# Performance work log

Measured on AMD Instinct MI355X. Metric: run time of the kernel, lower is better.

Reference implementation:

```python
import jax, jax.numpy as jnp
import numpy as np

N = 20000      # nodes
E = 320000     # edges (before self-loops)
F_IN = 50      # PPI num_features
C1 = 256       # per-head channels, conv1/conv2
H1 = 4         # heads, conv1/conv2
C3 = 121       # PPI num_classes, conv3 per-head channels
H3 = 6         # heads, conv3 (concat=False -> mean)


def gat_conv(x, src, dst, W, a_src, a_dst, b, heads, ch, concat, n):
    """PyG-style GATConv with self-loops already included in (src, dst).
    Messages flow src -> dst; softmax is over incoming edges of each dst node."""
    h = (x @ W).reshape(n, heads, ch)                      # [N, H, C]
    es = jnp.sum(h * a_src, axis=-1)                       # [N, H]
    ed = jnp.sum(h * a_dst, axis=-1)                       # [N, H]
    e = jax.nn.leaky_relu(es[src] + ed[dst], 0.2)          # [E', H]
    m = jax.ops.segment_max(e, dst, num_segments=n)        # stable softmax per dst
    e = jnp.exp(e - m[dst])
    denom = jax.ops.segment_sum(e, dst, num_segments=n)
    alpha = e / jnp.maximum(denom[dst], 1e-16)             # [E', H]
    out = jax.ops.segment_sum(alpha[:, :, None] * h[src], dst, num_segments=n)  # [N, H, C]
    out = out.reshape(n, heads * ch) if concat else out.mean(axis=1)
    return out + b


def setup_inputs() -> dict:
    key = jax.random.key(0)
    ks = jax.random.split(key, 16)

    def p(k, shape, fan_in):
        return (jax.random.normal(k, shape, jnp.float32) / np.float32(np.sqrt(fan_in)))

    x = jax.random.normal(ks[0], (N, F_IN), jnp.float32)
    edge_index = jax.random.randint(ks[1], (2, E), 0, N, dtype=jnp.int64)
    D1 = H1 * C1  # 1024
    return dict(
        x=x, edge_index=edge_index,
        W1=p(ks[2], (F_IN, D1), F_IN), a1s=p(ks[3], (H1, C1), C1), a1d=p(ks[4], (H1, C1), C1), b1=jnp.zeros((D1,), jnp.float32),
        Wl1=p(ks[5], (F_IN, D1), F_IN), bl1=jnp.zeros((D1,), jnp.float32),
        W2=p(ks[6], (D1, D1), D1), a2s=p(ks[7], (H1, C1), C1), a2d=p(ks[8], (H1, C1), C1), b2=jnp.zeros((D1,), jnp.float32),
        Wl2=p(ks[9], (D1, D1), D1), bl2=jnp.zeros((D1,), jnp.float32),
        W3=p(ks[10], (D1, H3 * C3), D1), a3s=p(ks[11], (H3, C3), C3), a3d=p(ks[12], (H3, C3), C3), b3=jnp.zeros((C3,), jnp.float32),
        Wl3=p(ks[13], (D1, C3), D1), bl3=jnp.zeros((C3,), jnp.float32),
    )


def reference(x, edge_index, W1, a1s, a1d, b1, Wl1, bl1, W2, a2s, a2d, b2, Wl2, bl2, W3, a3s, a3d, b3, Wl3, bl3):
    n = x.shape[0]
    loop = jnp.arange(n, dtype=edge_index.dtype)           # PyG GATConv adds self-loops
    src = jnp.concatenate([edge_index[0], loop])
    dst = jnp.concatenate([edge_index[1], loop])
    x1 = jax.nn.elu(gat_conv(x, src, dst, W1, a1s, a1d, b1, H1, C1, True, n) + x @ Wl1 + bl1)
    x2 = jax.nn.elu(gat_conv(x1, src, dst, W2, a2s, a2d, b2, H1, C1, True, n) + x1 @ Wl2 + bl2)
    out = gat_conv(x2, src, dst, W3, a3s, a3d, b3, H3, C3, False, n) + x2 @ Wl3 + bl3
    return out
```

## Files before the change

kernel.cpp:

```cpp
#include <hip/hip_runtime.h>
#include <hip/hip_bf16.h>
#include <math.h>

typedef __bf16 bf16;
typedef __attribute__((ext_vector_type(4))) __bf16 bf16x4;
typedef __attribute__((ext_vector_type(8))) __bf16 bf16x8;
typedef __attribute__((ext_vector_type(4))) float f32x4;

#define N_NODES 20000
#define N_EDGES 320000
#define E2 (N_EDGES + N_NODES)
#define F_IN 50
#define D1 1024
#define NP12 2048
#define NP3 1024
#define SG 2048
#define KA 320

#define PO_A1S 0
#define PO_A1D 1024
#define PO_B1  2048
#define PO_BL1 3072
#define PO_A2S 4096
#define PO_A2D 5120
#define PO_B2  6144
#define PO_BL2 7168
#define PO_A3S 8192
#define PO_A3D 8918
#define PO_B3  9644
#define PO_BL3 9765
#define PO_END 9886

__device__ __forceinline__ int clampi(int v, int lo, int hi)
{
    return v < lo ? lo : (v > hi ? hi : v);
}

__device__ __forceinline__ float loadf(const void* p, long idx, int isb)
{
    return isb ? (float)((const bf16*)p)[idx] : ((const float*)p)[idx];
}

__device__ __forceinline__ int loadei(const int* ei, long idx, int i64)
{
    return i64 ? ei[2 * idx] : ei[idx];
}

__global__ void k_detect(const int* __restrict__ ei,
                         const unsigned short* __restrict__ xw,
                         int* __restrict__ flags)
{
    if (blockIdx.x != 0 || threadIdx.x != 0) return;
    int allz = 1;
    for (int i = 0; i < 128; ++i)
        if (ei[2 * i + 1] != 0) { allz = 0; break; }
    int inr = 0;
    for (int i = 0; i < 128; ++i) {
        int e = (xw[2 * i] >> 7) & 0xFF;
        if (e >= 100 && e <= 140) inr++;
    }
    flags[0] = allz;
    flags[1] = (inr >= 64) ? 1 : 0;
}

template <bool BACT>
__global__ __launch_bounds__(256) void k_gemm(const bf16* __restrict__ A,
                                              const bf16* __restrict__ Bt,
                                              bf16* __restrict__ C,
                                              int M, int K, int lda, int ldb, int ldc,
                                              int mtiles, int ntiles,
                                              const bf16* __restrict__ bias)
{
    __shared__ bf16 As[128 * 64];
    __shared__ bf16 Bs[128 * 64];

    int id = blockIdx.x;
    int gfull = mtiles >> 3;
    int base  = gfull * 8 * ntiles;
    int x, y;
    if (id < base) {
        int gsz = 8 * ntiles;
        int g = id / gsz;
        int r = id - g * gsz;
        x = g * 8 + (r & 7);
        y = r >> 3;
    } else {
        int rem = mtiles - (gfull << 3);
        int r = id - base;
        x = (gfull << 3) + r % rem;
        y = r / rem;
    }
    const int m0 = x * 128;
    const int n0 = y * 128;

    const int tid  = threadIdx.x;
    const int wave = tid >> 6;
    const int lane = tid & 63;
    const int wm   = (wave >> 1) * 64;
    const int wn   = (wave & 1) * 64;
    const int frow  = lane & 15;

    const int srow = wave * 32 + (lane >> 3);
    const int scol = (((lane & 7) ^ (lane >> 3)) * 8);

    f32x4 acc[4][4];
#pragma unroll
    for (int i = 0; i < 4; ++i)
#pragma unroll
        for (int j = 0; j < 4; ++j)
#pragma unroll
            for (int r = 0; r < 4; ++r) acc[i][j][r] = 0.f;

    for (int k0 = 0; k0 < K; k0 += 64) {
#pragma unroll
        for (int i = 0; i < 4; ++i) {
            int ra = srow + i * 8;
            int ga = m0 + ra; if (ga > M - 1) ga = M - 1;
            __builtin_amdgcn_global_load_lds(
                (const __attribute__((address_space(1))) void*)(A + (size_t)ga * lda + k0 + scol),
                (__attribute__((address_space(3))) void*)(As + wave * 2048 + i * 512),
                16, 0, 0);
            int gb = n0 + ra;
            __builtin_amdgcn_global_load_lds(
                (const __attribute__((address_space(1))) void*)(Bt + (size_t)gb * ldb + k0 + scol),
                (__attribute__((address_space(3))) void*)(Bs + wave * 2048 + i * 512),
                16, 0, 0);
        }
        __syncthreads();
#pragma unroll
        for (int kk = 0; kk < 2; ++kk) {
            const int coff = (((kk * 4 + (lane >> 4)) ^ (frow & 7)) << 3);
            bf16x8 af[4], bfr[4];
#pragma unroll
            for (int i = 0; i < 4; ++i) {
                af[i]  = *(const bf16x8*)(As + (wm + i * 16 + frow) * 64 + coff);
                bfr[i] = *(const bf16x8*)(Bs + (wn + i * 16 + frow) * 64 + coff);
            }
#pragma unroll
            for (int i = 0; i < 4; ++i)
#pragma unroll
                for (int j = 0; j < 4; ++j)
                    acc[i][j] = __builtin_amdgcn_mfma_f32_16x16x32_bf16(af[i], bfr[j], acc[i][j], 0, 0, 0);
        }
        __syncthreads();
    }

#pragma unroll
    for (int i = 0; i < 4; ++i) {
#pragma unroll
        for (int j = 0; j < 4; ++j) {
            int rbase = m0 + wm + i * 16 + (lane >> 4) * 4;
            int col   = n0 + wn + j * 16 + frow;
            if constexpr (BACT) {
                float bv = (float)bias[col];
#pragma unroll
                for (int r = 0; r < 4; ++r) {
                    int row = rbase + r;
                    if (row < M) {
                        float v = acc[i][j][r] + bv;
                        v = (v > 0.f) ? v : (__expf(v) - 1.f);
                        C[(size_t)row * ldc + col] = (bf16)v;
                    }
                }
            } else {
#pragma unroll
                for (int r = 0; r < 4; ++r) {
                    int row = rbase + r;
                    if (row < M) C[(size_t)row * ldc + col] = (bf16)acc[i][j][r];
                }
            }
        }
    }
}

__global__ __launch_bounds__(512, 2) void k_gemm256(const bf16* __restrict__ A,
                                                    const bf16* __restrict__ Bt,
                                                    bf16* __restrict__ C,
                                                    int M, int K, int lda, int ldb, int ldc,
                                                    int mtiles, int ntiles)
{
    __shared__ bf16 As[2][256 * 64];
    __shared__ bf16 Bs[2][256 * 64];

    int id = blockIdx.x;
    int gfull = mtiles >> 3;
    int base  = gfull * 8 * ntiles;
    int x, y;
    if (id < base) {
        int gsz = 8 * ntiles;
        int g = id / gsz;
        int r = id - g * gsz;
        x = g * 8 + (r & 7);
        y = r >> 3;
    } else {
        int rem = mtiles - (gfull << 3);
        int r = id - base;
        x = (gfull << 3) + r % rem;
        y = r / rem;
    }
    const int m0 = x * 256;
    const int n0 = y * 256;

    const int tid  = threadIdx.x;
    const int wave = tid >> 6;
    const int lane = tid & 63;
    const int wr   = wave >> 2;
    const int wc   = wave & 3;
    const int frow = lane & 15;
    const int hi   = lane >> 4;
    const int sr8  = lane >> 3;
    const int scol = (((lane & 7) ^ sr8) << 3);

    auto stage_a = [&](int b, int h, int t1) {
        const int k0s = t1 << 6;
#pragma unroll
        for (int i_ = 0; i_ < 2; ++i_) {
            int row_ = h * 128 + i_ * 64 + wave * 8 + sr8;
            int ga_ = m0 + row_; if (ga_ > M - 1) ga_ = M - 1;
            __builtin_amdgcn_global_load_lds(
                (const __attribute__((address_space(1))) void*)(A + (size_t)ga_ * lda + k0s + scol),
                (__attribute__((address_space(3))) void*)(&As[b][(h * 128 + i_ * 64 + wave * 8) * 64]),
                16, 0, 0);
        }
    };
    auto stage_b = [&](int b, int h, int t1) {
        const int k0s = t1 << 6;
#pragma unroll
        for (int i_ = 0; i_ < 2; ++i_) {
            int row_ = h * 128 + i_ * 64 + wave * 8 + sr8;
            int gb_ = n0 + row_;
            __builtin_amdgcn_global_load_lds(
                (const __attribute__((address_space(1))) void*)(Bt + (size_t)gb_ * ldb + k0s + scol),
                (__attribute__((address_space(3))) void*)(&Bs[b][(h * 128 + i_ * 64 + wave * 8) * 64]),
                16, 0, 0);
        }
    };

    f32x4 acc[8][4];
#pragma unroll
    for (int i = 0; i < 8; ++i)
#pragma unroll
        for (int j = 0; j < 4; ++j)
#pragma unroll
            for (int r = 0; r < 4; ++r) acc[i][j][r] = 0.f;

    auto compute = [&](int b, int MH, int NH) {
        bf16x8 af[4][2], bv[2][2];
#pragma unroll
        for (int m_ = 0; m_ < 4; ++m_)
#pragma unroll
            for (int kk_ = 0; kk_ < 2; ++kk_)
                af[m_][kk_] = *(const bf16x8*)&As[b][
                    (wr * 128 + MH * 64 + m_ * 16 + frow) * 64 +
                    (((kk_ * 4 + hi) ^ (frow & 7)) << 3)];
#pragma unroll
        for (int n_ = 0; n_ < 2; ++n_)
#pragma unroll
            for (int kk_ = 0; kk_ < 2; ++kk_)
                bv[n_][kk_] = *(const bf16x8*)&Bs[b][
                    (wc * 64 + NH * 32 + n_ * 16 + frow) * 64 +
                    (((kk_ * 4 + hi) ^ (frow & 7)) << 3)];
        __builtin_amdgcn_s_setprio(1);
#pragma unroll
        for (int kk_ = 0; kk_ < 2; ++kk_)
#pragma unroll
            for (int m_ = 0; m_ < 4; ++m_)
#pragma unroll
                for (int n_ = 0; n_ < 2; ++n_)
                    acc[MH * 4 + m_][NH * 2 + n_] =
                        __builtin_amdgcn_mfma_f32_16x16x32_bf16(
                            af[m_][kk_], bv[n_][kk_],
                            acc[MH * 4 + m_][NH * 2 + n_], 0, 0, 0);
        __builtin_amdgcn_s_setprio(0);
    };

    stage_a(0, 0, 0);
    stage_b(0, 0, 0);
    stage_b(0, 1, 0);
    stage_a(0, 1, 0);

    const int nt = K >> 6;
    int p = 0;
#pragma unroll 1
    for (int t = 0; t < nt - 1; ++t, p ^= 1) {
        stage_a(p ^ 1, 0, t + 1);
        asm volatile("s_waitcnt vmcnt(2)" ::: "memory");
        __builtin_amdgcn_s_barrier();
        compute(p, 0, 0);
        __builtin_amdgcn_s_barrier();
        stage_b(p ^ 1, 0, t + 1);
        compute(p, 0, 1);
        __builtin_amdgcn_s_barrier();
        stage_b(p ^ 1, 1, t + 1);
        compute(p, 1, 1);
        __builtin_amdgcn_s_barrier();
        stage_a(p ^ 1, 1, t + 1);
        compute(p, 1, 0);
        __builtin_amdgcn_s_barrier();
    }
    asm volatile("s_waitcnt vmcnt(0)" ::: "memory");
    __builtin_amdgcn_s_barrier();
    compute(p, 0, 0);
    compute(p, 0, 1);
    compute(p, 1, 1);
    compute(p, 1, 0);

#pragma unroll
    for (int mf = 0; mf < 8; ++mf) {
#pragma unroll
        for (int nf = 0; nf < 4; ++nf) {
            int row0 = m0 + wr * 128 + mf * 16 + hi * 4;
            int col  = n0 + wc * 64 + nf * 16 + frow;
#pragma unroll
            for (int r = 0; r < 4; ++r) {
                int row = row0 + r;
                if (row < M) C[(size_t)row * ldc + col] = (bf16)acc[mf][nf][r];
            }
        }
    }
}

__global__ void k_padx(const void* __restrict__ x, bf16* __restrict__ A2,
                       const int* __restrict__ flags)
{
    int idx = blockIdx.x * 256 + threadIdx.x;
    if (idx >= N_NODES * 64) return;
    int isb = flags[1];
    int n = idx >> 6, k = idx & 63;
    A2[(size_t)n * KA + 256 + k] = (k < F_IN) ? (bf16)loadf(x, (long)n * F_IN + k, isb)
                                              : (bf16)0.f;
}

__global__ __launch_bounds__(256) void k_veca(const void* __restrict__ W1,
                                              const void* __restrict__ a1s,
                                              const void* __restrict__ a1d,
                                              const void* __restrict__ b1,
                                              const void* __restrict__ bl1,
                                              float* __restrict__ ws, float* __restrict__ wd,
                                              bf16* __restrict__ bsum,
                                              const int* __restrict__ flags)
{
    const int isb = flags[1];
    const int k = blockIdx.x;
    const int h = threadIdx.x >> 6;
    const int c0 = threadIdx.x & 63;
    float s = 0.f, d = 0.f;
    if (k < F_IN) {
        for (int c = c0; c < 256; c += 64) {
            float wv = loadf(W1, (long)k * D1 + h * 256 + c, isb);
            s += wv * loadf(a1s, h * 256 + c, isb);
            d += wv * loadf(a1d, h * 256 + c, isb);
        }
    }
#pragma unroll
    for (int off = 32; off; off >>= 1) {
        s += __shfl_xor(s, off);
        d += __shfl_xor(d, off);
    }
    if (c0 == 0) { ws[k * 4 + h] = s; wd[k * 4 + h] = d; }
    if (k < 4) {
        int j = k * 256 + threadIdx.x;
        bsum[j] = (bf16)(loadf(b1, j, isb) + loadf(bl1, j, isb));
    }
}

__global__ void k_wfuse1(const void* __restrict__ W1, const void* __restrict__ Wl1,
                         bf16* __restrict__ Bt, const int* __restrict__ flags)
{
    int idx = blockIdx.x * 256 + threadIdx.x;
    if (idx >= D1 * KA) return;
    int isb = flags[1];
    int j = idx / KA;
    int kp = idx - j * KA;
    float v = 0.f;
    if (kp < 256) {
        int hp = kp >> 6, k = kp & 63;
        if ((j >> 8) == hp && k < F_IN) v = loadf(W1, (long)k * D1 + j, isb);
    } else {
        int k = kp - 256;
        if (k < F_IN) v = loadf(Wl1, (long)k * D1 + j, isb);
    }
    Bt[idx] = (bf16)v;
}

__global__ __launch_bounds__(256) void k_wcatT(const void* __restrict__ Wa,
                                               const void* __restrict__ Wb,
                                               bf16* __restrict__ Bt,
                                               int split, int da, int db,
                                               const int* __restrict__ flags)
{
    __shared__ bf16 T[64][65];
    const int isb = flags[1];
    const int k0 = blockIdx.x * 64;
    const int n0 = blockIdx.y * 64;
    const int r = threadIdx.x >> 6;
    const int c = threadIdx.x & 63;
    const int n = n0 + c;
#pragma unroll
    for (int kk = 0; kk < 16; ++kk) {
        int k = k0 + r + kk * 4;
        float v = 0.f;
        if (n < split)           v = loadf(Wa, (long)k * da + n, isb);
        else if (n < split + db) v = loadf(Wb, (long)k * db + (n - split), isb);
        T[r + kk * 4][c] = (bf16)v;
    }
    __syncthreads();
#pragma unroll
    for (int kk = 0; kk < 16; ++kk) {
        int nn = r + kk * 4;
        Bt[(size_t)(n0 + nn) * 1024 + k0 + c] = T[c][nn];
    }
}

struct P12 { const void* s[12]; };

__global__ void k_params(P12 ps, bf16* __restrict__ pool, const int* __restrict__ flags)
{
    const int off[13] = {PO_A1S, PO_A1D, PO_B1, PO_BL1, PO_A2S, PO_A2D, PO_B2,
                         PO_BL2, PO_A3S, PO_A3D, PO_B3, PO_BL3, PO_END};
    int idx = blockIdx.x * 256 + threadIdx.x;
    if (idx >= PO_END) return;
    int isb = flags[1];
    int seg = 0;
    while (idx >= off[seg + 1]) seg++;
    pool[idx] = (bf16)loadf(ps.s[seg], idx - off[seg], isb);
}

__global__ void k_count(const int* __restrict__ ei, int* __restrict__ cnt,
                        const int* __restrict__ flags)
{
    int e = blockIdx.x * 256 + threadIdx.x;
    if (e >= E2) return;
    int i64 = flags[0];
    int d = (e < N_EDGES) ? loadei(ei, (long)N_EDGES + e, i64) : (e - N_EDGES);
    d = clampi(d, 0, N_NODES - 1);
    atomicAdd(&cnt[d], 1);
}

__global__ __launch_bounds__(256) void k_scan(const int* __restrict__ cnt, int* __restrict__ rp)
{
    __shared__ int ssum[256];
    int tid = threadIdx.x;
    const int chunk = (N_NODES + 255) / 256;
    int lo = tid * chunk;
    int hi = lo + chunk; if (hi > N_NODES) hi = N_NODES;
    int s = 0;
    for (int i = lo; i < hi; ++i) s += cnt[i];
    ssum[tid] = s;
    __syncthreads();
    if (tid == 0) {
        int run = 0;
        for (int i = 0; i < 256; ++i) { int t = ssum[i]; ssum[i] = run; run += t; }
        rp[N_NODES] = run;
    }
    __syncthreads();
    int run = ssum[tid];
    for (int i = lo; i < hi; ++i) { rp[i] = run; run += cnt[i]; }
}

__global__ void k_copy(const int* __restrict__ rp, int* __restrict__ cur)
{
    int i = blockIdx.x * 256 + threadIdx.x;
    if (i < N_NODES) cur[i] = rp[i];
}

__global__ void k_fill(const int* __restrict__ ei, int* __restrict__ cur,
                       int* __restrict__ ss, const int* __restrict__ flags)
{
    int e = blockIdx.x * 256 + threadIdx.x;
    if (e >= E2) return;
    int i64 = flags[0];
    int s, d;
    if (e < N_EDGES) {
        s = loadei(ei, e, i64);
        d = loadei(ei, (long)N_EDGES + e, i64);
    } else {
        s = e - N_EDGES; d = s;
    }
    s = clampi(s, 0, N_NODES - 1);
    d = clampi(d, 0, N_NODES - 1);
    int pos = atomicAdd(&cur[d], 1);
    if (pos >= 0 && pos < E2) ss[pos] = s;
}

__global__ __launch_bounds__(256) void k_logits1(const bf16* __restrict__ A2,
                                                 const float* __restrict__ ws,
                                                 const float* __restrict__ wd,
                                                 float* __restrict__ es, float* __restrict__ ed)
{
    const int wave = threadIdx.x >> 6;
    const int lane = threadIdx.x & 63;
    const int n = blockIdx.x * 4 + wave;
    if (n >= N_NODES) return;
    float xv = (float)A2[(size_t)n * KA + 256 + lane];
    f32x4 wsv = *(const f32x4*)(ws + lane * 4);
    f32x4 wdv = *(const f32x4*)(wd + lane * 4);
    float s[4], d[4];
#pragma unroll
    for (int h = 0; h < 4; ++h) { s[h] = xv * wsv[h]; d[h] = xv * wdv[h]; }
#pragma unroll
    for (int off = 32; off; off >>= 1)
#pragma unroll
        for (int h = 0; h < 4; ++h) {
            s[h] += __shfl_xor(s[h], off);
            d[h] += __shfl_xor(d[h], off);
        }
    if (lane == 0) {
#pragma unroll
        for (int h = 0; h < 4; ++h) { es[n * 4 + h] = s[h]; ed[n * 4 + h] = d[h]; }
    }
}

__global__ __launch_bounds__(256) void k_aggx(bf16* __restrict__ A2,
                                              const float* __restrict__ es,
                                              const float* __restrict__ ed,
                                              const int* __restrict__ rp,
                                              const int* __restrict__ ss)
{
    __shared__ float smx[4], sinv[4], sed[4];
    __shared__ float sal[64 * 4];
    __shared__ int   ssrc[64];

    const int n   = blockIdx.x;
    const int tid = threadIdx.x;
    int r0 = clampi(rp[n], 0, E2);
    int r1 = clampi(rp[n + 1], r0, E2);
    const int deg = r1 - r0;

    const int sw = tid >> 5, ln = tid & 31;
    if (sw < 4) {
        int h = sw;
        float edn = ed[n * 4 + h];
        float mx = -1e30f;
        for (int e = ln; e < deg; e += 32) {
            int s = clampi(ss[r0 + e], 0, N_NODES - 1);
            float w = es[s * 4 + h] + edn;
            w = (w > 0.f) ? w : 0.2f * w;
            mx = fmaxf(mx, w);
        }
#pragma unroll
        for (int off = 16; off; off >>= 1) mx = fmaxf(mx, __shfl_xor(mx, off, 32));
        float sm = 0.f;
        for (int e = ln; e < deg; e += 32) {
            int s = clampi(ss[r0 + e], 0, N_NODES - 1);
            float w = es[s * 4 + h] + edn;
            w = (w > 0.f) ? w : 0.2f * w;
            sm += __expf(w - mx);
        }
#pragma unroll
        for (int off = 16; off; off >>= 1) sm += __shfl_xor(sm, off, 32);
        if (ln == 0) { smx[h] = mx; sinv[h] = 1.f / fmaxf(sm, 1e-16f); sed[h] = edn; }
    }
    __syncthreads();

    const int k  = tid & 63;
    const int hh = tid >> 6;
    float acc = 0.f;

    for (int e0 = 0; e0 < deg; e0 += 64) {
        int ce = min(64, deg - e0);
        int ce4 = (ce + 3) & ~3;
        __syncthreads();
        if (tid < ce4 * 4) {
            int e = tid >> 2, h = tid & 3;
            int valid = (e < ce);
            int s = valid ? clampi(ss[r0 + e0 + e], 0, N_NODES - 1) : 0;
            float w = es[s * 4 + h] + sed[h];
            w = (w > 0.f) ? w : 0.2f * w;
            sal[e * 4 + h] = valid ? __expf(w - smx[h]) * sinv[h] : 0.f;
            if (h == 0) ssrc[e] = s;
        }
        __syncthreads();
        for (int e = 0; e < ce4; e += 4) {
            float xv[4], al[4];
#pragma unroll
            for (int p = 0; p < 4; ++p) {
                int s = ssrc[e + p];
                xv[p] = (float)A2[(size_t)s * KA + 256 + k];
            }
#pragma unroll
            for (int p = 0; p < 4; ++p) al[p] = sal[(e + p) * 4 + hh];
#pragma unroll
            for (int p = 0; p < 4; ++p) acc += al[p] * xv[p];
        }
    }
    A2[(size_t)n * KA + hh * 64 + k] = (bf16)acc;
}

template <int H, int C>
__global__ __launch_bounds__(256) void k_logits(const bf16* __restrict__ G,
                                                const bf16* __restrict__ as_,
                                                const bf16* __restrict__ ad_,
                                                float* __restrict__ es, float* __restrict__ ed)
{
    const int wave = threadIdx.x >> 6;
    const int lane = threadIdx.x & 63;
    const int n = blockIdx.x * 4 + wave;
    if (n >= N_NODES) return;

#pragma unroll
    for (int h = 0; h < H; ++h) {
        float s = 0.f, d = 0.f;
        if constexpr (C == 256) {
            bf16x4 g  = *(const bf16x4*)(G + (size_t)n * SG + h * 256 + lane * 4);
            bf16x4 av = *(const bf16x4*)(as_ + h * 256 + lane * 4);
            bf16x4 dv = *(const bf16x4*)(ad_ + h * 256 + lane * 4);
#pragma unroll
            for (int j = 0; j < 4; ++j) {
                float gv = (float)g[j];
                s += gv * (float)av[j];
                d += gv * (float)dv[j];
            }
        } else {
            for (int c = lane; c < C; c += 64) {
                float hv = (float)G[(size_t)n * SG + h * C + c];
                s += hv * (float)as_[h * C + c];
                d += hv * (float)ad_[h * C + c];
            }
        }
#pragma unroll
        for (int off = 32; off; off >>= 1) {
            s += __shfl_xor(s, off);
            d += __shfl_xor(d, off);
        }
        if (lane == 0) { es[n * H + h] = s; ed[n * H + h] = d; }
    }
}

template <int H, int C, bool MEAN, bool ELU, bool EXTOUT>
__global__ __launch_bounds__(256) void k_agg(const bf16* __restrict__ G,
                                             const bf16* __restrict__ S,
                                             const float* __restrict__ es,
                                             const float* __restrict__ ed,
                                             const int* __restrict__ rp,
                                             const int* __restrict__ ss,
                                             const bf16* __restrict__ bgat,
                                             const bf16* __restrict__ bskip,
                                             void* __restrict__ out, int sout,
                                             const int* __restrict__ flags)
{
    constexpr int D  = H * C;
    constexpr int NV = (D + 3) / 4;
    constexpr int CH = 256;
    __shared__ float smx[H], sinv[H], sed[H];
    __shared__ float sal[CH * H];
    __shared__ int   ssrc[CH];

    const int n   = blockIdx.x;
    const int tid = threadIdx.x;
    int r0 = clampi(rp[n], 0, E2);
    int r1 = clampi(rp[n + 1], r0, E2);
    const int deg = r1 - r0;

    const int sw = tid >> 5, ln = tid & 31;
    for (int h = sw; h < H; h += 8) {
        float edn = ed[n * H + h];
        float mx = -1e30f;
        for (int e = ln; e < deg; e += 32) {
            int s = clampi(ss[r0 + e], 0, N_NODES - 1);
            float w = es[s * H + h] + edn;
            w = (w > 0.f) ? w : 0.2f * w;
            mx = fmaxf(mx, w);
        }
#pragma unroll
        for (int off = 16; off; off >>= 1) mx = fmaxf(mx, __shfl_xor(mx, off, 32));
        float sm = 0.f;
        for (int e = ln; e < deg; e += 32) {
            int s = clampi(ss[r0 + e], 0, N_NODES - 1);
            float w = es[s * H + h] + edn;
            w = (w > 0.f) ? w : 0.2f * w;
            sm += __expf(w - mx);
        }
#pragma unroll
        for (int off = 16; off; off >>= 1) sm += __shfl_xor(sm, off, 32);
        if (ln == 0) { smx[h] = mx; sinv[h] = 1.f / fmaxf(sm, 1e-16f); sed[h] = edn; }
    }
    __syncthreads();

    const int c0 = tid * 4;
    const int hA = (c0 < D) ? (c0 / C) : 0;
    const int hB = (c0 + 3 < D) ? ((c0 + 3) / C) : hA;
    int hj1 = ((c0 + 1 < D) ? ((c0 + 1) / C) : hA) == hA;
    int hj2 = ((c0 + 2 < D) ? ((c0 + 2) / C) : hA) == hA;
    const bool active = (tid < NV);

    float acc[4] = {0.f, 0.f, 0.f, 0.f};

    for (int e0 = 0; e0 < deg; e0 += CH) {
        int ce = min(CH, deg - e0);
        int ce4 = (ce + 3) & ~3;
        __syncthreads();
        for (int t = tid; t < ce4 * H; t += 256) {
            int e = t / H, h = t - e * H;
            int valid = (e < ce);
            int s = valid ? clampi(ss[r0 + e0 + e], 0, N_NODES - 1) : 0;
            float w = es[s * H + h] + sed[h];
            w = (w > 0.f) ? w : 0.2f * w;
            sal[e * H + h] = valid ? __expf(w - smx[h]) * sinv[h] : 0.f;
            if (h == 0) ssrc[e] = s;
        }
        __syncthreads();
        if (active) {
            for (int eb = 0; eb < ce4; eb += 4) {
                int sg[4];
#pragma unroll
                for (int p = 0; p < 4; ++p) sg[p] = ssrc[eb + p];
                bf16x4 g[4];
#pragma unroll
                for (int p = 0; p < 4; ++p)
                    g[p] = *(const bf16x4*)(G + (size_t)sg[p] * SG + c0);
                if constexpr (C % 4 == 0) {
                    float a[4];
#pragma unroll
                    for (int p = 0; p < 4; ++p) a[p] = sal[(eb + p) * H + hA];
#pragma unroll
                    for (int p = 0; p < 4; ++p)
#pragma unroll
                        for (int j = 0; j < 4; ++j)
                            acc[j] += a[p] * (float)g[p][j];
                } else {
#pragma unroll
                    for (int p = 0; p < 4; ++p) {
                        float aL = sal[(eb + p) * H + hA];
                        float aH = sal[(eb + p) * H + hB];
                        acc[0] += aL * (float)g[p][0];
                        acc[1] += (hj1 ? aL : aH) * (float)g[p][1];
                        acc[2] += (hj2 ? aL : aH) * (float)g[p][2];
                        acc[3] += aH * (float)g[p][3];
                    }
                }
            }
        }
    }

    const int outbf = EXTOUT ? flags[1] : 1;

    if constexpr (!MEAN) {
        if (active) {
            bf16x4 bg = *(const bf16x4*)(bgat + c0);
            bf16x4 sk = *(const bf16x4*)(S + (size_t)n * SG + c0);
            bf16x4 bs = *(const bf16x4*)(bskip + c0);
            bf16x4 ov;
#pragma unroll
            for (int j = 0; j < 4; ++j) {
                float v = acc[j] + (float)bg[j] + (float)sk[j] + (float)bs[j];
                if (ELU) v = (v > 0.f) ? v : (__expf(v) - 1.f);
                ov[j] = (bf16)v;
            }
            *(bf16x4*)((bf16*)out + (size_t)n * sout + c0) = ov;
        }
    } else {
        __shared__ float sagg[D];
        if (active) {
#pragma unroll
            for (int j = 0; j < 4; ++j) {
                int c = c0 + j;
                if (c < D) sagg[c] = acc[j];
            }
        }
        __syncthreads();
        for (int c = tid; c < C; c += 256) {
            float v = 0.f;
#pragma unroll
            for (int h = 0; h < H; ++h) v += sagg[h * C + c];
            v *= (1.f / H);
            v += (float)bgat[c] + (float)S[(size_t)n * SG + c] + (float)bskip[c];
            if (outbf) ((bf16*)out)[(size_t)n * sout + c] = (bf16)v;
            else       ((float*)out)[(size_t)n * sout + c] = v;
        }
    }
}

extern "C" void kernel_launch(void* const* d_in, const int* in_sizes, int n_in,
                              void* d_out, int out_size, void* d_ws, size_t ws_size,
                              hipStream_t stream)
{
    const void* x   = d_in[0];
    const int*  ei  = (const int*)d_in[1];
    const void* W1  = d_in[2];
    const void* Wl1 = d_in[6];
    const void* W2  = d_in[8];
    const void* Wl2 = d_in[12];
    const void* W3  = d_in[14];
    const void* Wl3 = d_in[18];

    P12 ps;
    ps.s[0] = d_in[3];  ps.s[1] = d_in[4];  ps.s[2] = d_in[5];  ps.s[3] = d_in[7];
    ps.s[4] = d_in[9];  ps.s[5] = d_in[10]; ps.s[6] = d_in[11]; ps.s[7] = d_in[13];
    ps.s[8] = d_in[15]; ps.s[9] = d_in[16]; ps.s[10] = d_in[17]; ps.s[11] = d_in[19];

    char* w = (char*)d_ws;
    auto alloc = [&](size_t bytes) {
        char* p = w;
        w += (bytes + 255) & ~(size_t)255;
        return p;
    };
    int*   flags = (int*)alloc(64);
    int*   cnt   = (int*)alloc((size_t)N_NODES * 4);
    int*   rp    = (int*)alloc((size_t)(N_NODES + 1) * 4);
    int*   cur   = (int*)alloc((size_t)N_NODES * 4);
    int*   ss    = (int*)alloc((size_t)E2 * 4);
    float* es    = (float*)alloc((size_t)N_NODES * 6 * 4);
    float* ed    = (float*)alloc((size_t)N_NODES * 6 * 4);
    bf16*  pool  = (bf16*)alloc((size_t)PO_END * 2);
    float* ws1   = (float*)alloc((size_t)64 * 4 * 4);
    float* wd1   = (float*)alloc((size_t)64 * 4 * 4);
    bf16*  bsum  = (bf16*)alloc((size_t)D1 * 2);
    bf16*  Bt    = (bf16*)alloc((size_t)NP12 * 1024 * 2);
    bf16*  X     = (bf16*)alloc((size_t)N_NODES * D1 * 2);
    bf16*  WS    = (bf16*)alloc((size_t)N_NODES * SG * 2);
    bf16*  A2    = WS;

    k_detect<<<1, 64, 0, stream>>>(ei, (const unsigned short*)x, flags);

    hipMemsetAsync(cnt, 0, N_NODES * 4, stream);
    k_count<<<(E2 + 255) / 256, 256, 0, stream>>>(ei, cnt, flags);
    k_scan<<<1, 256, 0, stream>>>(cnt, rp);
    k_copy<<<(N_NODES + 255) / 256, 256, 0, stream>>>(rp, cur);
    k_fill<<<(E2 + 255) / 256, 256, 0, stream>>>(ei, cur, ss, flags);

    k_params<<<(PO_END + 255) / 256, 256, 0, stream>>>(ps, pool, flags);

    const dim3 blk(256);
    const int MT  = (N_NODES + 127) / 128;
    const int MT2 = (N_NODES + 255) / 256;

    k_veca<<<64, 256, 0, stream>>>(W1, ps.s[0], ps.s[1], ps.s[2], ps.s[3],
                                   ws1, wd1, bsum, flags);
    k_padx<<<(N_NODES * 64 + 255) / 256, 256, 0, stream>>>(x, A2, flags);
    k_wfuse1<<<(D1 * KA + 255) / 256, 256, 0, stream>>>(W1, Wl1, Bt, flags);
    k_logits1<<<N_NODES / 4, 256, 0, stream>>>(A2, ws1, wd1, es, ed);
    k_aggx<<<N_NODES, 256, 0, stream>>>(A2, es, ed, rp, ss);
    k_gemm<true><<<MT * (D1 / 128), blk, 0, stream>>>(A2, Bt, X, N_NODES, KA, KA, KA, D1,
                                                      MT, D1 / 128, bsum);

    k_wcatT<<<dim3(16, NP12 / 64), blk, 0, stream>>>(W2, Wl2, Bt, 1024, 1024, 1024, flags);
    k_gemm256<<<MT2 * (NP12 / 256), 512, 0, stream>>>(X, Bt, WS, N_NODES, 1024, 1024, 1024, SG,
                                                      MT2, NP12 / 256);
    k_logits<4, 256><<<N_NODES / 4, 256, 0, stream>>>(WS, pool + PO_A2S, pool + PO_A2D, es, ed);
    k_agg<4, 256, false, true, false><<<N_NODES, 256, 0, stream>>>(
        WS, WS + D1, es, ed, rp, ss, pool + PO_B2, pool + PO_BL2, X, D1, flags);

    k_wcatT<<<dim3(16, NP3 / 64), blk, 0, stream>>>(W3, Wl3, Bt, 726, 726, 121, flags);
    k_gemm256<<<MT2 * (NP3 / 256), 512, 0, stream>>>(X, Bt, WS, N_NODES, 1024, 1024, 1024, SG,
                                                     MT2, NP3 / 256);
    k_logits<6, 121><<<N_NODES / 4, 256, 0, stream>>>(WS, pool + PO_A3S, pool + PO_A3D, es, ed);
    k_agg<6, 121, true, false, true><<<N_NODES, 256, 0, stream>>>(
        WS, WS + 726, es, ed, rp, ss, pool + PO_B3, pool + PO_BL3, d_out, 121, flags);
}
```

Before: 733.0 us.

## Deepen k_gemm256 load pipelining and merge small prep kernels into one launch

The 256-tile GEMM now issues each next-stage global load before the compute that follows it, with finer vmcnt waits and fewer barriers per K step, so loads overlap MFMA work. The warp-to-subtile mapping also changes so each quarter-tile compute step touches a distinct staged LDS region. Separately, padx, wfuse1, params and logits1 are fused into a single k_prep launch, logits1 now reads x directly, and the rp→cur copy is folded into the scan. These cut launch overhead and barrier stalls, at the cost of more outstanding loads and a staging order that must exactly match the wait counts.

After: 695.9 us. 1.05x faster.

```diff
diff --git a/kernel.cpp b/kernel.cpp
--- a/kernel.cpp
+++ b/kernel.cpp
@@ -30,6 +30,11 @@
 #define PO_B3  9644
 #define PO_BL3 9765
 #define PO_END 9886
+
+#define PB_PADX  5000
+#define PB_WF1   1280
+#define PB_PAR   39
+#define PB_LOG1  5000
 
 __device__ __forceinline__ int clampi(int v, int lo, int hi)
 {
@@ -251,14 +256,14 @@
 #pragma unroll
             for (int kk_ = 0; kk_ < 2; ++kk_)
                 af[m_][kk_] = *(const bf16x8*)&As[b][
-                    (wr * 128 + MH * 64 + m_ * 16 + frow) * 64 +
+                    (MH * 128 + wr * 64 + m_ * 16 + frow) * 64 +
                     (((kk_ * 4 + hi) ^ (frow & 7)) << 3)];
 #pragma unroll
         for (int n_ = 0; n_ < 2; ++n_)
 #pragma unroll
             for (int kk_ = 0; kk_ < 2; ++kk_)
                 bv[n_][kk_] = *(const bf16x8*)&Bs[b][
-                    (wc * 64 + NH * 32 + n_ * 16 + frow) * 64 +
+                    (NH * 128 + wc * 32 + n_ * 16 + frow) * 64 +
                     (((kk_ * 4 + hi) ^ (frow & 7)) << 3)];
         __builtin_amdgcn_s_setprio(1);
 #pragma unroll
@@ -284,24 +289,28 @@
 #pragma unroll 1
     for (int t = 0; t < nt - 1; ++t, p ^= 1) {
         stage_a(p ^ 1, 0, t + 1);
-        asm volatile("s_waitcnt vmcnt(2)" ::: "memory");
+        asm volatile("s_waitcnt vmcnt(6)" ::: "memory");
         __builtin_amdgcn_s_barrier();
         compute(p, 0, 0);
+        stage_b(p ^ 1, 0, t + 1);
+        asm volatile("s_waitcnt vmcnt(6)" ::: "memory");
         __builtin_amdgcn_s_barrier();
-        stage_b(p ^ 1, 0, t + 1);
         compute(p, 0, 1);
+        stage_b(p ^ 1, 1, t + 1);
+        asm volatile("s_waitcnt vmcnt(6)" ::: "memory");
         __builtin_amdgcn_s_barrier();
-        stage_b(p ^ 1, 1, t + 1);
         compute(p, 1, 1);
-        __builtin_amdgcn_s_barrier();
         stage_a(p ^ 1, 1, t + 1);
         compute(p, 1, 0);
-        __builtin_amdgcn_s_barrier();
-    }
+    }
+    asm volatile("s_waitcnt vmcnt(4)" ::: "memory");
+    __builtin_amdgcn_s_barrier();
+    compute(p, 0, 0);
+    asm volatile("s_waitcnt vmcnt(2)" ::: "memory");
+    __builtin_amdgcn_s_barrier();
+    compute(p, 0, 1);
     asm volatile("s_waitcnt vmcnt(0)" ::: "memory");
     __builtin_amdgcn_s_barrier();
-    compute(p, 0, 0);
-    compute(p, 0, 1);
     compute(p, 1, 1);
     compute(p, 1, 0);
 
@@ -309,8 +318,8 @@
     for (int mf = 0; mf < 8; ++mf) {
 #pragma unroll
         for (int nf = 0; nf < 4; ++nf) {
-            int row0 = m0 + wr * 128 + mf * 16 + hi * 4;
-            int col  = n0 + wc * 64 + nf * 16 + frow;
+            int row0 = m0 + (mf >> 2) * 128 + wr * 64 + (mf & 3) * 16 + hi * 4;
+            int col  = n0 + (nf >> 1) * 128 + wc * 32 + (nf & 1) * 16 + frow;
 #pragma unroll
             for (int r = 0; r < 4; ++r) {
                 int row = row0 + r;
@@ -318,17 +327,6 @@
             }
         }
     }
-}
-
-__global__ void k_padx(const void* __restrict__ x, bf16* __restrict__ A2,
-                       const int* __restrict__ flags)
-{
-    int idx = blockIdx.x * 256 + threadIdx.x;
-    if (idx >= N_NODES * 64) return;
-    int isb = flags[1];
-    int n = idx >> 6, k = idx & 63;
-    A2[(size_t)n * KA + 256 + k] = (k < F_IN) ? (bf16)loadf(x, (long)n * F_IN + k, isb)
-                                              : (bf16)0.f;
 }
 
 __global__ __launch_bounds__(256) void k_veca(const void* __restrict__ W1,
@@ -364,23 +362,84 @@
     }
 }
 
-__global__ void k_wfuse1(const void* __restrict__ W1, const void* __restrict__ Wl1,
-                         bf16* __restrict__ Bt, const int* __restrict__ flags)
-{
-    int idx = blockIdx.x * 256 + threadIdx.x;
-    if (idx >= D1 * KA) return;
-    int isb = flags[1];
-    int j = idx / KA;
-    int kp = idx - j * KA;
-    float v = 0.f;
-    if (kp < 256) {
-        int hp = kp >> 6, k = kp & 63;
-        if ((j >> 8) == hp && k < F_IN) v = loadf(W1, (long)k * D1 + j, isb);
-    } else {
-        int k = kp - 256;
-        if (k < F_IN) v = loadf(Wl1, (long)k * D1 + j, isb);
-    }
-    Bt[idx] = (bf16)v;
+struct P12 { const void* s[12]; };
+
+__global__ __launch_bounds__(256) void k_prep(const void* __restrict__ x,
+                                              const void* __restrict__ W1,
+                                              const void* __restrict__ Wl1,
+                                              P12 ps,
+                                              bf16* __restrict__ A2,
+                                              bf16* __restrict__ Bt,
+                                              bf16* __restrict__ pool,
+                                              const float* __restrict__ ws,
+                                              const float* __restrict__ wd,
+                                              float* __restrict__ es,
+                                              float* __restrict__ ed,
+                                              const int* __restrict__ flags)
+{
+    const int isb = flags[1];
+    int b = blockIdx.x;
+
+    if (b < PB_PADX) {
+        int idx = b * 256 + threadIdx.x;
+        int n = idx >> 6, k = idx & 63;
+        A2[(size_t)n * KA + 256 + k] = (k < F_IN) ? (bf16)loadf(x, (long)n * F_IN + k, isb)
+                                                  : (bf16)0.f;
+        return;
+    }
+    b -= PB_PADX;
+
+    if (b < PB_WF1) {
+        int idx = b * 256 + threadIdx.x;
+        int j = idx / KA;
+        int kp = idx - j * KA;
+        float v = 0.f;
+        if (kp < 256) {
+            int hp = kp >> 6, k = kp & 63;
+            if ((j >> 8) == hp && k < F_IN) v = loadf(W1, (long)k * D1 + j, isb);
+        } else {
+            int k = kp - 256;
+            if (k < F_IN) v = loadf(Wl1, (long)k * D1 + j, isb);
+        }
+        Bt[idx] = (bf16)v;
+        return;
+    }
+    b -= PB_WF1;
+
+    if (b < PB_PAR) {
+        const int off[13] = {PO_A1S, PO_A1D, PO_B1, PO_BL1, PO_A2S, PO_A2D, PO_B2,
+                             PO_BL2, PO_A3S, PO_A3D, PO_B3, PO_BL3, PO_END};
+        int idx = b * 256 + threadIdx.x;
+        if (idx < PO_END) {
+            int seg = 0;
+            while (idx >= off[seg + 1]) seg++;
+            pool[idx] = (bf16)loadf(ps.s[seg], idx - off[seg], isb);
+        }
+        return;
+    }
+    b -= PB_PAR;
+
+    const int wave = threadIdx.x >> 6;
+    const int lane = threadIdx.x & 63;
+    const int n = b * 4 + wave;
+    if (n >= N_NODES) return;
+    float xv = (lane < F_IN) ? loadf(x, (long)n * F_IN + lane, isb) : 0.f;
+    f32x4 wsv = *(const f32x4*)(ws + lane * 4);
+    f32x4 wdv = *(const f32x4*)(wd + lane * 4);
+    float s[4], d[4];
+#pragma unroll
+    for (int h = 0; h < 4; ++h) { s[h] = xv * wsv[h]; d[h] = xv * wdv[h]; }
+#pragma unroll
+    for (int off = 32; off; off >>= 1)
+#pragma unroll
+        for (int h = 0; h < 4; ++h) {
+            s[h] += __shfl_xor(s[h], off);
+            d[h] += __shfl_xor(d[h], off);
+        }
+    if (lane == 0) {
+#pragma unroll
+        for (int h = 0; h < 4; ++h) { es[n * 4 + h] = s[h]; ed[n * 4 + h] = d[h]; }
+    }
 }
 
 __global__ __launch_bounds__(256) void k_wcatT(const void* __restrict__ Wa,
@@ -412,20 +471,6 @@
     }
 }
 
-struct P12 { const void* s[12]; };
-
-__global__ void k_params(P12 ps, bf16* __restrict__ pool, const int* __restrict__ flags)
-{
-    const int off[13] = {PO_A1S, PO_A1D, PO_B1, PO_BL1, PO_A2S, PO_A2D, PO_B2,
-                         PO_BL2, PO_A3S, PO_A3D, PO_B3, PO_BL3, PO_END};
-    int idx = blockIdx.x * 256 + threadIdx.x;
-    if (idx >= PO_END) return;
-    int isb = flags[1];
-    int seg = 0;
-    while (idx >= off[seg + 1]) seg++;
-    pool[idx] = (bf16)loadf(ps.s[seg], idx - off[seg], isb);
-}
-
 __global__ void k_count(const int* __restrict__ ei, int* __restrict__ cnt,
                         const int* __restrict__ flags)
 {
@@ -437,7 +482,9 @@
     atomicAdd(&cnt[d], 1);
 }
 
-__global__ __launch_bounds__(256) void k_scan(const int* __restrict__ cnt, int* __restrict__ rp)
+__global__ __launch_bounds__(256) void k_scan(const int* __restrict__ cnt,
+                                              int* __restrict__ rp,
+                                              int* __restrict__ cur)
 {
     __shared__ int ssum[256];
     int tid = threadIdx.x;
@@ -455,13 +502,7 @@
     }
     __syncthreads();
     int run = ssum[tid];
-    for (int i = lo; i < hi; ++i) { rp[i] = run; run += cnt[i]; }
-}
-
-__global__ void k_copy(const int* __restrict__ rp, int* __restrict__ cur)
-{
-    int i = blockIdx.x * 256 + threadIdx.x;
-    if (i < N_NODES) cur[i] = rp[i];
+    for (int i = lo; i < hi; ++i) { rp[i] = run; cur[i] = run; run += cnt[i]; }
 }
 
 __global__ void k_fill(const int* __restrict__ ei, int* __restrict__ cur,
@@ -481,34 +522,6 @@
     d = clampi(d, 0, N_NODES - 1);
     int pos = atomicAdd(&cur[d], 1);
     if (pos >= 0 && pos < E2) ss[pos] = s;
-}
-
-__global__ __launch_bounds__(256) void k_logits1(const bf16* __restrict__ A2,
-                                                 const float* __restrict__ ws,
-                                                 const float* __restrict__ wd,
-                                                 float* __restrict__ es, float* __restrict__ ed)
-{
-    const int wave = threadIdx.x >> 6;
-    const int lane = threadIdx.x & 63;
-    const int n = blockIdx.x * 4 + wave;
-    if (n >= N_NODES) return;
-    float xv = (float)A2[(size_t)n * KA + 256 + lane];
-    f32x4 wsv = *(const f32x4*)(ws + lane * 4);
-    f32x4 wdv = *(const f32x4*)(wd + lane * 4);
-    float s[4], d[4];
-#pragma unroll
-    for (int h = 0; h < 4; ++h) { s[h] = xv * wsv[h]; d[h] = xv * wdv[h]; }
-#pragma unroll
-    for (int off = 32; off; off >>= 1)
-#pragma unroll
-        for (int h = 0; h < 4; ++h) {
-            s[h] += __shfl_xor(s[h], off);
-            d[h] += __shfl_xor(d[h], off);
-        }
-    if (lane == 0) {
-#pragma unroll
-        for (int h = 0; h < 4; ++h) { es[n * 4 + h] = s[h]; ed[n * 4 + h] = d[h]; }
-    }
 }
 
 __global__ __launch_bounds__(256) void k_aggx(bf16* __restrict__ A2,
@@ -815,11 +828,8 @@
 
     hipMemsetAsync(cnt, 0, N_NODES * 4, stream);
     k_count<<<(E2 + 255) / 256, 256, 0, stream>>>(ei, cnt, flags);
-    k_scan<<<1, 256, 0, stream>>>(cnt, rp);
-    k_copy<<<(N_NODES + 255) / 256, 256, 0, stream>>>(rp, cur);
+    k_scan<<<1, 256, 0, stream>>>(cnt, rp, cur);
     k_fill<<<(E2 + 255) / 256, 256, 0, stream>>>(ei, cur, ss, flags);
-
-    k_params<<<(PO_END + 255) / 256, 256, 0, stream>>>(ps, pool, flags);
 
     const dim3 blk(256);
     const int MT  = (N_NODES + 127) / 128;
@@ -827,9 +837,8 @@
 
     k_veca<<<64, 256, 0, stream>>>(W1, ps.s[0], ps.s[1], ps.s[2], ps.s[3],
                                    ws1, wd1, bsum, flags);
-    k_padx<<<(N_NODES * 64 + 255) / 256, 256, 0, stream>>>(x, A2, flags);
-    k_wfuse1<<<(D1 * KA + 255) / 256, 256, 0, stream>>>(W1, Wl1, Bt, flags);
-    k_logits1<<<N_NODES / 4, 256, 0, stream>>>(A2, ws1, wd1, es, ed);
+    k_prep<<<PB_PADX + PB_WF1 + PB_PAR + PB_LOG1, 256, 0, stream>>>(
+        x, W1, Wl1, ps, A2, Bt, pool, ws1, wd1, es, ed, flags);
     k_aggx<<<N_NODES, 256, 0, stream>>>(A2, es, ed, rp, ss);
     k_gemm<true><<<MT * (D1 / 128), blk, 0, stream>>>(A2, Bt, X, N_NODES, KA, KA, KA, D1,
                                                       MT, D1 / 128, bsum);
```
